# Kernel tuning notes

Hardware: AMD Instinct MI355X
Metric: run time of the kernel (lower is better)

Reference implementation:

```python
import jax, jax.numpy as jnp
import numpy as np

EMBED_DIM = 1024
ATTN_DIM = 128
B, S = 4, 2048


def setup_inputs() -> dict:
    key = jax.random.key(0)
    k1, k2, k3, k4 = jax.random.split(key, 4)
    embedded = jax.random.normal(k1, (B, S, EMBED_DIM), dtype=jnp.float32)
    # torch nn.Linear weights are [out_features, in_features]
    scale = 1.0 / np.sqrt(EMBED_DIM)
    Wk = jax.random.uniform(k2, (ATTN_DIM, EMBED_DIM), dtype=jnp.float32, minval=-scale, maxval=scale)
    Wq = jax.random.uniform(k3, (ATTN_DIM, EMBED_DIM), dtype=jnp.float32, minval=-scale, maxval=scale)
    Wv = jax.random.uniform(k4, (ATTN_DIM, EMBED_DIM), dtype=jnp.float32, minval=-scale, maxval=scale)
    return {"embedded": embedded, "Wk": Wk, "Wq": Wq, "Wv": Wv}


def reference(embedded, Wk, Wq, Wv):
    # projections (no bias): x @ W.T
    k = jnp.einsum('bse,ae->bsa', embedded, Wk)  # [B,S,A]
    q = jnp.einsum('bse,ae->bsa', embedded, Wq)
    v = jnp.einsum('bse,ae->bsa', embedded, Wv)
    ad = k.shape[-1]
    scores = jnp.einsum('bqa,bka->bqk', q, k) / jnp.sqrt(jnp.float32(ad))  # [B,S,S]
    causal = jnp.tril(jnp.ones((scores.shape[1], scores.shape[1]), dtype=bool))
    scores = jnp.where(causal, scores, -jnp.inf)
    probs = jax.nn.softmax(scores, axis=-1)
    out = jnp.einsum('bqk,bka->bqa', probs, v)
    return jnp.round(out, 4)
```

## Files before the change

### kernel.cpp

```cpp
#include <hip/hip_runtime.h>
#include <hip/hip_bf16.h>
#include <math.h>

#define B 4
#define S 2048
#define E 1024
#define A 128
#define CHUNK 256
#define NCHMAX 8

typedef __attribute__((ext_vector_type(8))) short short8;
typedef __attribute__((ext_vector_type(4))) float floatx4;

static __device__ __forceinline__ short f2bf(float f) {
  union { float f; unsigned u; } c;
  c.f = f;
  unsigned r = (c.u + 0x7fffu + ((c.u >> 16) & 1u)) >> 16;
  return (short)r;
}
static __device__ __forceinline__ unsigned f2bf2(float x, float y) {
  __hip_bfloat162 h = __float22bfloat162_rn(float2{x, y});
  union { __hip_bfloat162 h; unsigned u; } c;
  c.h = h;
  return c.u;
}

__global__ __launch_bounds__(256) void wconv(
    const float* __restrict__ Wq,
    const float* __restrict__ Wk,
    const float* __restrict__ Wv,
    short* __restrict__ Wbf) {
  const int which = blockIdx.y;
  const float* Wp = (which == 0) ? Wq : (which == 1) ? Wk : Wv;
  short* o = Wbf + (size_t)which * A * E;
  const int f = blockIdx.x * 256 + threadIdx.x;
  const float4 v = *(const float4*)&Wp[(size_t)f * 4];
  uint2 p; p.x = f2bf2(v.x, v.y); p.y = f2bf2(v.z, v.w);
  *(uint2*)&o[(size_t)f * 4] = p;
}

__global__ __launch_bounds__(256) void proj_gemm(
    const float* __restrict__ X,
    const short* __restrict__ Wbf,
    short* __restrict__ Qbf,
    short* __restrict__ Kbf,
    short* __restrict__ Vt) {
  __shared__ short As[64 * 64];
  __shared__ short Bs[128 * 64];

  const int m0 = blockIdx.x * 64;
  const int which = blockIdx.y;
  const short* Wpb = Wbf + (size_t)which * A * E;

  const int tid = threadIdx.x;
  const int wave = tid >> 6;
  const int lane = tid & 63;
  const int mh = wave & 1;
  const int nh = wave >> 1;
  const int l16 = lane & 15;
  const int quad = lane >> 4;

  int xbase[4], wbase[4], aoff[4], boff[4];
#pragma unroll
  for (int i = 0; i < 4; ++i) {
    const int fa = tid + i * 256;
    const int arow = fa >> 4, ac4 = fa & 15;
    xbase[i] = (m0 + arow) * E + ac4 * 4;
    aoff[i] = arow * 64 + (((ac4 >> 1) ^ (arow & 7)) << 3) + ((ac4 & 1) << 2);
    const int fb = tid + i * 256;
    const int brow = fb >> 3, bc8 = fb & 7;
    wbase[i] = brow * E + bc8 * 8;
    boff[i] = brow * 64 + ((bc8 ^ (brow & 7)) << 3);
  }

  int arb[2], brb[4], swz[2];
#pragma unroll
  for (int ms = 0; ms < 2; ++ms) arb[ms] = (mh * 32 + ms * 16 + l16) * 64;
#pragma unroll
  for (int nt = 0; nt < 4; ++nt) brb[nt] = (nh * 64 + nt * 16 + l16) * 64;
#pragma unroll
  for (int ks = 0; ks < 2; ++ks) swz[ks] = (((ks * 4 + quad) ^ (l16 & 7)) << 3);

  floatx4 acc[2][4] = {};
  float4 apl0[4], apl1[4];
  short8 bpl0[4], bpl1[4];

#pragma unroll
  for (int i = 0; i < 4; ++i) {
    apl0[i] = *(const float4*)&X[xbase[i]];
    bpl0[i] = *(const short8*)&Wpb[wbase[i]];
    apl1[i] = *(const float4*)&X[xbase[i] + 64];
    bpl1[i] = *(const short8*)&Wpb[wbase[i] + 64];
  }

#define PROJ_BODY(APL, BPL, KNEXT)                                            \
  do {                                                                        \
    __syncthreads();                                                          \
    _Pragma("unroll") for (int i = 0; i < 4; ++i) {                           \
      uint2 pk; pk.x = f2bf2(APL[i].x, APL[i].y);                             \
      pk.y = f2bf2(APL[i].z, APL[i].w);                                       \
      *(uint2*)&As[aoff[i]] = pk;                                             \
      *(short8*)&Bs[boff[i]] = BPL[i];                                        \
    }                                                                         \
    __syncthreads();                                                          \
    if ((KNEXT) < E) {                                                        \
      _Pragma("unroll") for (int i = 0; i < 4; ++i) {                         \
        APL[i] = *(const float4*)&X[xbase[i] + (KNEXT)];                      \
        BPL[i] = *(const short8*)&Wpb[wbase[i] + (KNEXT)];                    \
      }                                                                       \
    }                                                                         \
    short8 afr[2][2], bfr[4][2];                                              \
    _Pragma("unroll") for (int ms = 0; ms < 2; ++ms)                          \
      _Pragma("unroll") for (int ks = 0; ks < 2; ++ks)                        \
        afr[ms][ks] = *(const short8*)&As[arb[ms] + swz[ks]];                 \
    _Pragma("unroll") for (int nt = 0; nt < 4; ++nt)                          \
      _Pragma("unroll") for (int ks = 0; ks < 2; ++ks)                        \
        bfr[nt][ks] = *(const short8*)&Bs[brb[nt] + swz[ks]];                 \
    _Pragma("unroll") for (int ms = 0; ms < 2; ++ms)                          \
      _Pragma("unroll") for (int nt = 0; nt < 4; ++nt)                        \
        _Pragma("unroll") for (int ks = 0; ks < 2; ++ks)                      \
          acc[ms][nt] = __builtin_amdgcn_mfma_f32_16x16x32_bf16(              \
              afr[ms][ks], bfr[nt][ks], acc[ms][nt], 0, 0, 0);                \
  } while (0)

  for (int k0 = 0; k0 < E; k0 += 128) {
    PROJ_BODY(apl0, bpl0, k0 + 128);
    PROJ_BODY(apl1, bpl1, k0 + 192);
  }
#undef PROJ_BODY

  const float qscale = 0.08838834764831845f;
#pragma unroll
  for (int ms = 0; ms < 2; ++ms) {
#pragma unroll
    for (int nt = 0; nt < 4; ++nt) {
      const int n = nh * 64 + nt * 16 + l16;
      const int mbase = m0 + mh * 32 + ms * 16 + quad * 4;
      if (which == 2) {
        const int b = mbase >> 11, s = mbase & (S - 1);
        short4 p;
        p.x = f2bf(acc[ms][nt][0]); p.y = f2bf(acc[ms][nt][1]);
        p.z = f2bf(acc[ms][nt][2]); p.w = f2bf(acc[ms][nt][3]);
        *(short4*)&Vt[((size_t)b * A + n) * S + s] = p;
      } else {
        short* Outp = (which == 0) ? Qbf : Kbf;
        const float sc = (which == 0) ? qscale : 1.0f;
#pragma unroll
        for (int r = 0; r < 4; ++r)
          Outp[(size_t)(mbase + r) * A + n] = f2bf(acc[ms][nt][r] * sc);
      }
    }
  }
}

__global__ __launch_bounds__(256) void attn_part(
    const short* __restrict__ Qbf,
    const short* __restrict__ Kbf,
    const short* __restrict__ Vt,
    float* __restrict__ Opart,
    float* __restrict__ Lpart) {
  __shared__ short Ks[64 * 128];
  __shared__ short Vs[128 * 64];
  __shared__ short Ps[4][16 * 64];

  const int rev = (int)gridDim.x - 1 - (int)blockIdx.x;
  const int qt = rev >> 3;
  const int chunk = rev & 7;
  const int b = qt >> 5;
  const int q0 = (qt & 31) << 6;
  const int nk = q0 + 64;
  const int kstart = chunk * CHUNK;
  if (kstart >= nk) return;
  const int kend = min(kstart + CHUNK, nk);

  const int tid = threadIdx.x;
  const int wave = tid >> 6;
  const int lane = tid & 63;
  const int l16 = lane & 15;
  const int quad = lane >> 4;

  int kgb[4], vgb[4], kwoff[4], vwoff[4];
#pragma unroll
  for (int i = 0; i < 4; ++i) {
    const int f = tid + i * 256;
    const int krow = f >> 4, kc8 = f & 15;
    kgb[i] = krow * A + kc8 * 8;
    kwoff[i] = krow * 128 + ((kc8 ^ (krow & 7)) << 3);
    const int vrow = f >> 3, vc8 = f & 7;
    vgb[i] = vrow * S + vc8 * 8;
    vwoff[i] = vrow * 64 + ((vc8 ^ (vrow & 7)) << 3);
  }

  int swz[4];
#pragma unroll
  for (int ks = 0; ks < 4; ++ks) swz[ks] = (((ks * 4 + quad) ^ (l16 & 7)) << 3);

  int pwoff[4][4];
#pragma unroll
  for (int nt = 0; nt < 4; ++nt)
#pragma unroll
    for (int r = 0; r < 4; ++r) {
      const int row = quad * 4 + r;
      const int slot = nt * 2 + (l16 >> 3);
      pwoff[nt][r] = row * 64 + ((slot ^ (row & 7)) << 3) + (l16 & 7);
    }

  short8 qfr[4];
  {
    const size_t qrow = (size_t)(b * S + q0 + wave * 16 + l16);
#pragma unroll
    for (int ks = 0; ks < 4; ++ks)
      qfr[ks] = *(const short8*)&Qbf[qrow * A + ks * 32 + quad * 8];
  }

  float l_acc[4] = {0.f, 0.f, 0.f, 0.f};
  floatx4 oacc[8] = {};

  const int myrow = q0 + wave * 16 + quad * 4;
  const short* Kbase = Kbf + (size_t)b * S * A;
  const short* Vbase = Vt + (size_t)b * A * S;

  short8 kplf[4], vplf[4];
#pragma unroll
  for (int i = 0; i < 4; ++i) {
    kplf[i] = *(const short8*)&Kbase[kstart * A + kgb[i]];
    vplf[i] = *(const short8*)&Vbase[vgb[i] + kstart];
  }

  for (int j0 = kstart; j0 < kend; j0 += 64) {
    __syncthreads();
#pragma unroll
    for (int i = 0; i < 4; ++i) {
      *(short8*)&Ks[kwoff[i]] = kplf[i];
      *(short8*)&Vs[vwoff[i]] = vplf[i];
    }
    __syncthreads();

    if (j0 + 64 < kend) {
#pragma unroll
      for (int i = 0; i < 4; ++i) {
        kplf[i] = *(const short8*)&Kbase[(j0 + 64) * A + kgb[i]];
        vplf[i] = *(const short8*)&Vbase[vgb[i] + j0 + 64];
      }
    }

    floatx4 sc[4];
#pragma unroll
    for (int nt = 0; nt < 4; ++nt) {
      floatx4 c = {};
#pragma unroll
      for (int ks = 0; ks < 4; ++ks) {
        const short8 bfr = *(const short8*)&Ks[(nt * 16 + l16) * 128 + swz[ks]];
        c = __builtin_amdgcn_mfma_f32_16x16x32_bf16(qfr[ks], bfr, c, 0, 0, 0);
      }
      sc[nt] = c;
    }

#pragma unroll
    for (int nt = 0; nt < 4; ++nt) {
      const int key = j0 + nt * 16 + l16;
#pragma unroll
      for (int r = 0; r < 4; ++r) {
        const float p = (key > myrow + r) ? 0.f : __expf(sc[nt][r]);
        sc[nt][r] = p;
        l_acc[r] += p;
      }
    }

#pragma unroll
    for (int nt = 0; nt < 4; ++nt)
#pragma unroll
      for (int r = 0; r < 4; ++r)
        Ps[wave][pwoff[nt][r]] = f2bf(sc[nt][r]);

    short8 pfr[2];
#pragma unroll
    for (int ks = 0; ks < 2; ++ks)
      pfr[ks] = *(const short8*)&Ps[wave][l16 * 64 + swz[ks]];

#pragma unroll
    for (int nt = 0; nt < 8; ++nt) {
#pragma unroll
      for (int ks = 0; ks < 2; ++ks) {
        const short8 vfr = *(const short8*)&Vs[(nt * 16 + l16) * 64 + swz[ks]];
        oacc[nt] = __builtin_amdgcn_mfma_f32_16x16x32_bf16(pfr[ks], vfr, oacc[nt], 0, 0, 0);
      }
    }
  }

  const int slot = qt * NCHMAX + chunk;
  float* op = Opart + (size_t)slot * 64 * 128;
  const int lr = wave * 16 + quad * 4;
#pragma unroll
  for (int nt = 0; nt < 8; ++nt)
#pragma unroll
    for (int r = 0; r < 4; ++r)
      op[(lr + r) * 128 + nt * 16 + l16] = oacc[nt][r];

#pragma unroll
  for (int r = 0; r < 4; ++r) {
    float l = l_acc[r];
    l += __shfl_xor(l, 1);
    l += __shfl_xor(l, 2);
    l += __shfl_xor(l, 4);
    l += __shfl_xor(l, 8);
    if (l16 == 0) Lpart[slot * 64 + lr + r] = l;
  }
}

__global__ __launch_bounds__(256) void attn_reduce(
    const float* __restrict__ Opart,
    const float* __restrict__ Lpart,
    float* __restrict__ Out) {
  const int qt = blockIdx.x >> 2;
  const int quarter = blockIdx.x & 3;
  const int b = qt >> 5;
  const int q0 = (qt & 31) << 6;
  const int nch = (q0 + 64 + CHUNK - 1) / CHUNK;

  const int tid = threadIdx.x;
  const int lr = quarter * 16 + (tid >> 4);
  const int c0 = (tid & 15) * 8;

  float ltot = 0.f;
  for (int c = 0; c < nch; ++c) ltot += Lpart[(qt * NCHMAX + c) * 64 + lr];
  const float inv = 1.f / ltot;

  float4 acc[2] = {};
  for (int c = 0; c < nch; ++c) {
    const float4* op = (const float4*)
        (Opart + ((size_t)(qt * NCHMAX + c) * 64 + lr) * 128 + c0);
#pragma unroll
    for (int i = 0; i < 2; ++i) {
      const float4 v = op[i];
      acc[i].x += v.x; acc[i].y += v.y; acc[i].z += v.z; acc[i].w += v.w;
    }
  }

  float4* o = (float4*)(Out + (size_t)(b * S + q0 + lr) * A + c0);
#pragma unroll
  for (int i = 0; i < 2; ++i) {
    float4 v = acc[i];
    v.x *= inv; v.y *= inv; v.z *= inv; v.w *= inv;
    o[i] = v;
  }
}

extern "C" void kernel_launch(void* const* d_in, const int* in_sizes, int n_in,
                              void* d_out, int out_size, void* d_ws, size_t ws_size,
                              hipStream_t stream) {
  const float* X  = (const float*)d_in[0];
  const float* Wk = (const float*)d_in[1];
  const float* Wq = (const float*)d_in[2];
  const float* Wv = (const float*)d_in[3];
  float* Out = (float*)d_out;

  const size_t qkv_elems = (size_t)B * S * A;
  short* Qbf = (short*)d_ws;
  short* Kbf = Qbf + qkv_elems;
  short* Vt  = Kbf + qkv_elems;
  float* Opart = (float*)(Vt + qkv_elems);
  float* Lpart = Opart + (size_t)1024 * 64 * 128;
  short* Wbf = (short*)(Lpart + (size_t)1024 * 64);

  wconv<<<dim3(A * E / 4 / 256, 3), 256, 0, stream>>>(Wq, Wk, Wv, Wbf);
  dim3 pgrid(B * S / 64, 3);
  proj_gemm<<<pgrid, 256, 0, stream>>>(X, Wbf, Qbf, Kbf, Vt);
  attn_part<<<(B * S / 64) * NCHMAX, 256, 0, stream>>>(Qbf, Kbf, Vt, Opart, Lpart);
  attn_reduce<<<B * S / 64 * 4, 256, 0, stream>>>(Opart, Lpart, Out);
}
```

Baseline: 121.8 us.

## Widen projection K-tile to 128 and split attention keys into 128-wide chunks

The projection GEMM now stages a 128-wide K slice per iteration with a single register prefetch buffer instead of two 64-wide ping-pong buffers, halving barrier pairs and widening the XOR swizzle to 16. Attention key chunks shrink from 256 to 128 with up to 16 chunks per query tile, giving more parallel blocks for the causal split-K pass. The partial-output workspace grows to match. Risks are larger LDS use lowering projection occupancy, more partials for the reduce step, and possible mismatch in unseen attn_reduce/slot indexing.

```diff
diff --git a/kernel.cpp b/kernel.cpp
--- a/kernel.cpp
+++ b/kernel.cpp
@@ -6,8 +6,9 @@
 #define S 2048
 #define E 1024
 #define A 128
-#define CHUNK 256
-#define NCHMAX 8
+#define CHUNK 128
+#define NCHMAX 16
+#define NSLOT 2048
 
 typedef __attribute__((ext_vector_type(8))) short short8;
 typedef __attribute__((ext_vector_type(4))) float floatx4;
@@ -45,8 +46,8 @@
     short* __restrict__ Qbf,
     short* __restrict__ Kbf,
     short* __restrict__ Vt) {
-  __shared__ short As[64 * 64];
-  __shared__ short Bs[128 * 64];
+  __shared__ short As[64 * 128];
+  __shared__ short Bs[128 * 128];
 
   const int m0 = blockIdx.x * 64;
   const int which = blockIdx.y;
@@ -60,74 +61,73 @@
   const int l16 = lane & 15;
   const int quad = lane >> 4;
 
-  int xbase[4], wbase[4], aoff[4], boff[4];
-#pragma unroll
-  for (int i = 0; i < 4; ++i) {
+  int xbase[8], aoff[8], wbase[8], boff[8];
+#pragma unroll
+  for (int i = 0; i < 8; ++i) {
     const int fa = tid + i * 256;
-    const int arow = fa >> 4, ac4 = fa & 15;
+    const int arow = fa >> 5, ac4 = fa & 31;
     xbase[i] = (m0 + arow) * E + ac4 * 4;
-    aoff[i] = arow * 64 + (((ac4 >> 1) ^ (arow & 7)) << 3) + ((ac4 & 1) << 2);
+    aoff[i] = arow * 128 + (((ac4 >> 1) ^ (arow & 15)) << 3) + ((ac4 & 1) << 2);
     const int fb = tid + i * 256;
-    const int brow = fb >> 3, bc8 = fb & 7;
+    const int brow = fb >> 4, bc8 = fb & 15;
     wbase[i] = brow * E + bc8 * 8;
-    boff[i] = brow * 64 + ((bc8 ^ (brow & 7)) << 3);
-  }
-
-  int arb[2], brb[4], swz[2];
-#pragma unroll
-  for (int ms = 0; ms < 2; ++ms) arb[ms] = (mh * 32 + ms * 16 + l16) * 64;
-#pragma unroll
-  for (int nt = 0; nt < 4; ++nt) brb[nt] = (nh * 64 + nt * 16 + l16) * 64;
-#pragma unroll
-  for (int ks = 0; ks < 2; ++ks) swz[ks] = (((ks * 4 + quad) ^ (l16 & 7)) << 3);
+    boff[i] = brow * 128 + ((bc8 ^ (brow & 15)) << 3);
+  }
+
+  int arb[2], brb[4], swz[4];
+#pragma unroll
+  for (int ms = 0; ms < 2; ++ms) arb[ms] = (mh * 32 + ms * 16 + l16) * 128;
+#pragma unroll
+  for (int nt = 0; nt < 4; ++nt) brb[nt] = (nh * 64 + nt * 16 + l16) * 128;
+#pragma unroll
+  for (int ks = 0; ks < 4; ++ks) swz[ks] = (((ks * 4 + quad) ^ l16) << 3);
 
   floatx4 acc[2][4] = {};
-  float4 apl0[4], apl1[4];
-  short8 bpl0[4], bpl1[4];
-
-#pragma unroll
-  for (int i = 0; i < 4; ++i) {
-    apl0[i] = *(const float4*)&X[xbase[i]];
-    bpl0[i] = *(const short8*)&Wpb[wbase[i]];
-    apl1[i] = *(const float4*)&X[xbase[i] + 64];
-    bpl1[i] = *(const short8*)&Wpb[wbase[i] + 64];
-  }
-
-#define PROJ_BODY(APL, BPL, KNEXT)                                            \
-  do {                                                                        \
-    __syncthreads();                                                          \
-    _Pragma("unroll") for (int i = 0; i < 4; ++i) {                           \
-      uint2 pk; pk.x = f2bf2(APL[i].x, APL[i].y);                             \
-      pk.y = f2bf2(APL[i].z, APL[i].w);                                       \
-      *(uint2*)&As[aoff[i]] = pk;                                             \
-      *(short8*)&Bs[boff[i]] = BPL[i];                                        \
-    }                                                                         \
-    __syncthreads();                                                          \
-    if ((KNEXT) < E) {                                                        \
-      _Pragma("unroll") for (int i = 0; i < 4; ++i) {                         \
-        APL[i] = *(const float4*)&X[xbase[i] + (KNEXT)];                      \
-        BPL[i] = *(const short8*)&Wpb[wbase[i] + (KNEXT)];                    \
-      }                                                                       \
-    }                                                                         \
-    short8 afr[2][2], bfr[4][2];                                              \
-    _Pragma("unroll") for (int ms = 0; ms < 2; ++ms)                          \
-      _Pragma("unroll") for (int ks = 0; ks < 2; ++ks)                        \
-        afr[ms][ks] = *(const short8*)&As[arb[ms] + swz[ks]];                 \
-    _Pragma("unroll") for (int nt = 0; nt < 4; ++nt)                          \
-      _Pragma("unroll") for (int ks = 0; ks < 2; ++ks)                        \
-        bfr[nt][ks] = *(const short8*)&Bs[brb[nt] + swz[ks]];                 \
-    _Pragma("unroll") for (int ms = 0; ms < 2; ++ms)                          \
-      _Pragma("unroll") for (int nt = 0; nt < 4; ++nt)                        \
-        _Pragma("unroll") for (int ks = 0; ks < 2; ++ks)                      \
-          acc[ms][nt] = __builtin_amdgcn_mfma_f32_16x16x32_bf16(              \
-              afr[ms][ks], bfr[nt][ks], acc[ms][nt], 0, 0, 0);                \
-  } while (0)
+  float4 apl[8];
+  short8 bpl[8];
+
+#pragma unroll
+  for (int i = 0; i < 8; ++i) {
+    apl[i] = *(const float4*)&X[xbase[i]];
+    bpl[i] = *(const short8*)&Wpb[wbase[i]];
+  }
 
   for (int k0 = 0; k0 < E; k0 += 128) {
-    PROJ_BODY(apl0, bpl0, k0 + 128);
-    PROJ_BODY(apl1, bpl1, k0 + 192);
-  }
-#undef PROJ_BODY
+    __syncthreads();
+#pragma unroll
+    for (int i = 0; i < 8; ++i) {
+      uint2 pk; pk.x = f2bf2(apl[i].x, apl[i].y);
+      pk.y = f2bf2(apl[i].z, apl[i].w);
+      *(uint2*)&As[aoff[i]] = pk;
+      *(short8*)&Bs[boff[i]] = bpl[i];
+    }
+    __syncthreads();
+
+    if (k0 + 128 < E) {
+#pragma unroll
+      for (int i = 0; i < 8; ++i) {
+        apl[i] = *(const float4*)&X[xbase[i] + k0 + 128];
+        bpl[i] = *(const short8*)&Wpb[wbase[i] + k0 + 128];
+      }
+    }
+
+#pragma unroll
+    for (int ks = 0; ks < 4; ++ks) {
+      short8 afr[2], bfr[4];
+#pragma unroll
+      for (int ms = 0; ms < 2; ++ms)
+        afr[ms] = *(const short8*)&As[arb[ms] + swz[ks]];
+#pragma unroll
+      for (int nt = 0; nt < 4; ++nt)
+        bfr[nt] = *(const short8*)&Bs[brb[nt] + swz[ks]];
+#pragma unroll
+      for (int ms = 0; ms < 2; ++ms)
+#pragma unroll
+        for (int nt = 0; nt < 4; ++nt)
+          acc[ms][nt] = __builtin_amdgcn_mfma_f32_16x16x32_bf16(
+              afr[ms], bfr[nt], acc[ms][nt], 0, 0, 0);
+    }
+  }
 
   const float qscale = 0.08838834764831845f;
 #pragma unroll
@@ -164,8 +164,8 @@
   __shared__ short Ps[4][16 * 64];
 
   const int rev = (int)gridDim.x - 1 - (int)blockIdx.x;
-  const int qt = rev >> 3;
-  const int chunk = rev & 7;
+  const int qt = rev >> 4;
+  const int chunk = rev & 15;
   const int b = qt >> 5;
   const int q0 = (qt & 31) << 6;
   const int nk = q0 + 64;
@@ -360,8 +360,8 @@
   short* Kbf = Qbf + qkv_elems;
   short* Vt  = Kbf + qkv_elems;
   float* Opart = (float*)(Vt + qkv_elems);
-  float* Lpart = Opart + (size_t)1024 * 64 * 128;
-  short* Wbf = (short*)(Lpart + (size_t)1024 * 64);
+  float* Lpart = Opart + (size_t)NSLOT * 64 * 128;
+  short* Wbf = (short*)(Lpart + (size_t)NSLOT * 64);
 
   wconv<<<dim3(A * E / 4 / 256, 3), 256, 0, stream>>>(Wq, Wk, Wv, Wbf);
   dim3 pgrid(B * S / 64, 3);
```

After: 129.6 us. 6.4% more time.

## Replace split-K attention with single-pass per-tile attention and fused normalization

Applied to the files above, without the earlier changes.

Drops the key-chunk split (8 chunks of 256 keys) and the separate reduction kernel. Each block now handles one 64-row query tile over its whole causal key range and writes normalized output directly. This removes the partial-output writes and reads, the reduce launch and the early-exit empty blocks. In exchange there are only 128 blocks with very unequal work (1 to 32 key tiles), which risks poor occupancy and load imbalance on a GPU with many CUs.

```diff
diff --git a/kernel.cpp b/kernel.cpp
--- a/kernel.cpp
+++ b/kernel.cpp
@@ -6,8 +6,6 @@
 #define S 2048
 #define E 1024
 #define A 128
-#define CHUNK 256
-#define NCHMAX 8
 
 typedef __attribute__((ext_vector_type(8))) short short8;
 typedef __attribute__((ext_vector_type(4))) float floatx4;
@@ -153,25 +151,20 @@
   }
 }
 
-__global__ __launch_bounds__(256) void attn_part(
+__global__ __launch_bounds__(256) void attn_full(
     const short* __restrict__ Qbf,
     const short* __restrict__ Kbf,
     const short* __restrict__ Vt,
-    float* __restrict__ Opart,
-    float* __restrict__ Lpart) {
+    float* __restrict__ Out) {
   __shared__ short Ks[64 * 128];
   __shared__ short Vs[128 * 64];
   __shared__ short Ps[4][16 * 64];
 
   const int rev = (int)gridDim.x - 1 - (int)blockIdx.x;
-  const int qt = rev >> 3;
-  const int chunk = rev & 7;
-  const int b = qt >> 5;
-  const int q0 = (qt & 31) << 6;
+  const int t = rev >> 2;
+  const int b = rev & 3;
+  const int q0 = t << 6;
   const int nk = q0 + 64;
-  const int kstart = chunk * CHUNK;
-  if (kstart >= nk) return;
-  const int kend = min(kstart + CHUNK, nk);
 
   const int tid = threadIdx.x;
   const int wave = tid >> 6;
@@ -223,11 +216,11 @@
   short8 kplf[4], vplf[4];
 #pragma unroll
   for (int i = 0; i < 4; ++i) {
-    kplf[i] = *(const short8*)&Kbase[kstart * A + kgb[i]];
-    vplf[i] = *(const short8*)&Vbase[vgb[i] + kstart];
-  }
-
-  for (int j0 = kstart; j0 < kend; j0 += 64) {
+    kplf[i] = *(const short8*)&Kbase[kgb[i]];
+    vplf[i] = *(const short8*)&Vbase[vgb[i]];
+  }
+
+  for (int j0 = 0; j0 < nk; j0 += 64) {
     __syncthreads();
 #pragma unroll
     for (int i = 0; i < 4; ++i) {
@@ -236,7 +229,7 @@
     }
     __syncthreads();
 
-    if (j0 + 64 < kend) {
+    if (j0 + 64 < nk) {
 #pragma unroll
       for (int i = 0; i < 4; ++i) {
         kplf[i] = *(const short8*)&Kbase[(j0 + 64) * A + kgb[i]];
@@ -288,15 +281,8 @@
     }
   }
 
-  const int slot = qt * NCHMAX + chunk;
-  float* op = Opart + (size_t)slot * 64 * 128;
   const int lr = wave * 16 + quad * 4;
-#pragma unroll
-  for (int nt = 0; nt < 8; ++nt)
-#pragma unroll
-    for (int r = 0; r < 4; ++r)
-      op[(lr + r) * 128 + nt * 16 + l16] = oacc[nt][r];
-
+  float inv4[4];
 #pragma unroll
   for (int r = 0; r < 4; ++r) {
     float l = l_acc[r];
@@ -304,46 +290,15 @@
     l += __shfl_xor(l, 2);
     l += __shfl_xor(l, 4);
     l += __shfl_xor(l, 8);
-    if (l16 == 0) Lpart[slot * 64 + lr + r] = l;
-  }
-}
-
-__global__ __launch_bounds__(256) void attn_reduce(
-    const float* __restrict__ Opart,
-    const float* __restrict__ Lpart,
-    float* __restrict__ Out) {
-  const int qt = blockIdx.x >> 2;
-  const int quarter = blockIdx.x & 3;
-  const int b = qt >> 5;
-  const int q0 = (qt & 31) << 6;
-  const int nch = (q0 + 64 + CHUNK - 1) / CHUNK;
-
-  const int tid = threadIdx.x;
-  const int lr = quarter * 16 + (tid >> 4);
-  const int c0 = (tid & 15) * 8;
-
-  float ltot = 0.f;
-  for (int c = 0; c < nch; ++c) ltot += Lpart[(qt * NCHMAX + c) * 64 + lr];
-  const float inv = 1.f / ltot;
-
-  float4 acc[2] = {};
-  for (int c = 0; c < nch; ++c) {
-    const float4* op = (const float4*)
-        (Opart + ((size_t)(qt * NCHMAX + c) * 64 + lr) * 128 + c0);
-#pragma unroll
-    for (int i = 0; i < 2; ++i) {
-      const float4 v = op[i];
-      acc[i].x += v.x; acc[i].y += v.y; acc[i].z += v.z; acc[i].w += v.w;
-    }
-  }
-
-  float4* o = (float4*)(Out + (size_t)(b * S + q0 + lr) * A + c0);
-#pragma unroll
-  for (int i = 0; i < 2; ++i) {
-    float4 v = acc[i];
-    v.x *= inv; v.y *= inv; v.z *= inv; v.w *= inv;
-    o[i] = v;
-  }
+    inv4[r] = 1.f / l;
+  }
+
+  float* o = Out + (size_t)(b * S + q0 + lr) * A;
+#pragma unroll
+  for (int nt = 0; nt < 8; ++nt)
+#pragma unroll
+    for (int r = 0; r < 4; ++r)
+      o[(size_t)r * A + nt * 16 + l16] = oacc[nt][r] * inv4[r];
 }
 
 extern "C" void kernel_launch(void* const* d_in, const int* in_sizes, int n_in,
@@ -359,13 +314,10 @@
   short* Qbf = (short*)d_ws;
   short* Kbf = Qbf + qkv_elems;
   short* Vt  = Kbf + qkv_elems;
-  float* Opart = (float*)(Vt + qkv_elems);
-  float* Lpart = Opart + (size_t)1024 * 64 * 128;
-  short* Wbf = (short*)(Lpart + (size_t)1024 * 64);
+  short* Wbf = Vt + qkv_elems;
 
   wconv<<<dim3(A * E / 4 / 256, 3), 256, 0, stream>>>(Wq, Wk, Wv, Wbf);
   dim3 pgrid(B * S / 64, 3);
   proj_gemm<<<pgrid, 256, 0, stream>>>(X, Wbf, Qbf, Kbf, Vt);
-  attn_part<<<(B * S / 64) * NCHMAX, 256, 0, stream>>>(Qbf, Kbf, Vt, Opart, Lpart);
-  attn_reduce<<<B * S / 64 * 4, 256, 0, stream>>>(Opart, Lpart, Out);
-}
+  attn_full<<<B * S / 64, 256, 0, stream>>>(Qbf, Kbf, Vt, Out);
+}
```

After: 133.3 us. 9.5% more time.
